# Performance work log

Hardware: AMD Instinct MI355X
Metric: run time of the kernel (lower is better)

The kernel has to match this reference:

```python
import jax, jax.numpy as jnp
import numpy as np
import math

B, L = 32, 1000
N_CHAR, EMB, D_MODEL, N_HEADS, PRED_HS, N_OUT = 256, 512, 512, 8, 512, 8
D_HEAD = D_MODEL // N_HEADS


def _pos_encoding(seq_len, d_model, dtype=jnp.float32):
    pos = jnp.arange(seq_len, dtype=dtype)[:, None]                      # [L,1]
    div = jnp.exp(jnp.arange(0, d_model, 2, dtype=dtype) * (-math.log(10000.0) / d_model))
    pe = jnp.zeros((seq_len, d_model), dtype=dtype)
    pe = pe.at[:, 0::2].set(jnp.sin(pos * div))
    pe = pe.at[:, 1::2].set(jnp.cos(pos * div))
    return pe                                                            # [L,D]


def setup_inputs() -> dict:
    key = jax.random.key(0)
    ks = jax.random.split(key, 12)
    def xavier(k, shape):
        fan_in, fan_out = shape[1], shape[0]
        lim = math.sqrt(6.0 / (fan_in + fan_out))
        return jax.random.uniform(k, shape, jnp.float32, -lim, lim)
    data = jax.random.randint(ks[0], (B, L), 0, N_CHAR, dtype=jnp.int64)
    lengths = jnp.clip(jax.random.randint(ks[1], (B,), 0, L, dtype=jnp.int64), 1, L)
    emb = jax.random.normal(ks[2], (N_CHAR, EMB), jnp.float32) * math.sqrt(2.0 / (N_CHAR + EMB))
    return {
        'data': data,
        'lengths': lengths,
        'emb': emb,
        'Wq': xavier(ks[3], (D_MODEL, EMB)), 'bq': jnp.zeros((D_MODEL,), jnp.float32),
        'Wk': xavier(ks[4], (D_MODEL, EMB)), 'bk': jnp.zeros((D_MODEL,), jnp.float32),
        'Wv': xavier(ks[5], (D_MODEL, EMB)), 'bv': jnp.zeros((D_MODEL,), jnp.float32),
        'W1': xavier(ks[6], (PRED_HS, D_MODEL)), 'b1': jnp.full((PRED_HS,), 0.01, jnp.float32),
        'W2': xavier(ks[7], (N_OUT, PRED_HS)), 'b2': jnp.full((N_OUT,), 0.01, jnp.float32),
    }


def reference(data, lengths, emb, Wq, bq, Wk, bk, Wv, bv, W1, b1, W2, b2):
    bs, seq = data.shape
    x = emb[data]                                              # [B,L,E]
    x = x + _pos_encoding(seq, x.shape[-1], x.dtype)[None]     # positional encoding
    # q/k/v projections -> [B,L,H,dh]
    q = (x @ Wq.T + bq).reshape(bs, seq, N_HEADS, D_HEAD)
    k = (x @ Wk.T + bk).reshape(bs, seq, N_HEADS, D_HEAD)
    v = (x @ Wv.T + bv).reshape(bs, seq, N_HEADS, D_HEAD)
    scale = 1.0 / math.sqrt(D_HEAD)
    score = jnp.einsum('bqhd,bkhd->bhqk', q, k) * scale        # [B,H,L,L]
    causal = jnp.tril(jnp.ones((seq, seq), dtype=bool))        # True = keep
    score = jnp.where(causal[None, None], score, -jnp.inf)
    attn = jax.nn.softmax(score, axis=-1)
    ctx = jnp.einsum('bhqk,bkhd->bqhd', attn, v).reshape(bs, seq, D_MODEL)
    # take hidden state at last valid position per sequence
    ctx_last = jnp.take_along_axis(ctx, (lengths - 1)[:, None, None].astype(jnp.int32), axis=1)[:, 0]  # [B,D]
    h = jax.nn.leaky_relu(ctx_last @ W1.T + b1)                # pred layer 1
    out = jax.nn.relu(h @ W2.T + b2)                           # [B,8]
    out = jnp.mean(out, axis=-1)                               # [B]
    return jax.nn.leaky_relu(out)
```

## Files before the change

### kernel.cpp

```cpp
#include <hip/hip_runtime.h>
#include <math.h>

#define BATCH   32
#define LSEQ    1000
#define LPAD    1024
#define NHEADS  8
#define DHEAD   64

typedef __attribute__((ext_vector_type(8))) short s8v;
typedef __attribute__((ext_vector_type(4))) float f4v;

__device__ __forceinline__ unsigned short f2bf(float f) {
  unsigned u = __builtin_bit_cast(unsigned, f);
  u += 0x7fffu + ((u >> 16) & 1u);
  return (unsigned short)(u >> 16);
}
__device__ __forceinline__ float bf2f(unsigned short h) {
  return __builtin_bit_cast(float, ((unsigned)h) << 16);
}
__device__ __forceinline__ void g2lds16(const void* g, void* l) {
  __builtin_amdgcn_global_load_lds((const __attribute__((address_space(1))) void*)g,
                                   (__attribute__((address_space(3))) void*)l,
                                   16, 0, 0);
}

__global__ __launch_bounds__(256) void prep_kernel(
    const float* __restrict__ Wk, const float* __restrict__ bk,
    const float* __restrict__ Wv, const float* __restrict__ bv,
    unsigned short* __restrict__ Bkv, float* __restrict__ bias_kv) {
  int idx = blockIdx.x * 256 + threadIdx.x;
  int off = idx * 4;
  const float* s = (off < 262144) ? (Wk + off) : (Wv + off - 262144);
  float4 v = *(const float4*)s;
  unsigned r0 = (unsigned)f2bf(v.x) | ((unsigned)f2bf(v.y) << 16);
  unsigned r1 = (unsigned)f2bf(v.z) | ((unsigned)f2bf(v.w) << 16);
  uint2 pk; pk.x = r0; pk.y = r1;
  *(uint2*)(Bkv + off) = pk;
  if (idx < 1024) bias_kv[idx] = (idx < 512) ? bk[idx] : bv[idx - 512];
}

__global__ __launch_bounds__(256) void build_x_kernel(
    const int* __restrict__ data, const int* __restrict__ lengths,
    const float* __restrict__ emb, unsigned short* __restrict__ X) {
  int t    = threadIdx.x;
  int row  = blockIdx.x * 4 + (t >> 6);
  int b    = row / 1000;
  int j    = row - b * 1000;
  int p    = lengths[b] - 1;
  if (j > p) return;
  int lane = t & 63;
  int e0   = lane * 8;
  int tok  = data[row];
  const float* ev = emb + (size_t)tok * 512 + e0;
  float4 a = *(const float4*)(ev);
  float4 c = *(const float4*)(ev + 4);
  float vals[8] = {a.x, a.y, a.z, a.w, c.x, c.y, c.z, c.w};
  #pragma unroll
  for (int i = 0; i < 8; i += 2) {
    int e = e0 + i;
    float dv  = __expf((float)e * (-9.210340371976184f / 512.0f));
    float arg = (float)j * dv;
    vals[i]     += __sinf(arg);
    vals[i + 1] += __cosf(arg);
  }
  unsigned w0 = (unsigned)f2bf(vals[0]) | ((unsigned)f2bf(vals[1]) << 16);
  unsigned w1 = (unsigned)f2bf(vals[2]) | ((unsigned)f2bf(vals[3]) << 16);
  unsigned w2 = (unsigned)f2bf(vals[4]) | ((unsigned)f2bf(vals[5]) << 16);
  unsigned w3 = (unsigned)f2bf(vals[6]) | ((unsigned)f2bf(vals[7]) << 16);
  uint4 pk; pk.x = w0; pk.y = w1; pk.z = w2; pk.w = w3;
  *(uint4*)(X + ((size_t)(b * LPAD + j)) * 512 + e0) = pk;
}

__global__ __launch_bounds__(256) void kv_gemm_kernel(
    const unsigned short* __restrict__ X, const unsigned short* __restrict__ Bkv,
    const float* __restrict__ bias_kv, const int* __restrict__ lengths,
    unsigned short* __restrict__ Ck, unsigned short* __restrict__ Cv) {
  int b    = blockIdx.z;
  int row0 = blockIdx.y * 128;
  int p    = lengths[b] - 1;
  if (row0 > p) return;
  int n0   = blockIdx.x * 128;

  __shared__ unsigned short lA[128 * 64];
  __shared__ unsigned short lB[128 * 64];

  int t = threadIdx.x;
  int w = t >> 6;
  int lane = t & 63;
  int wm = w & 1, wn = w >> 1;

  f4v acc[4][4];
  f4v z = {0.0f, 0.0f, 0.0f, 0.0f};
  #pragma unroll
  for (int i = 0; i < 4; ++i)
    #pragma unroll
    for (int jn = 0; jn < 4; ++jn) acc[i][jn] = z;

  const unsigned short* gA[4];
  const unsigned short* gB[4];
  #pragma unroll
  for (int i = 0; i < 4; ++i) {
    int chunk = (i * 4 + w) * 64 + lane;
    int r  = chunk >> 3;
    int cc = (chunk & 7) ^ (r & 7);
    gA[i] = X   + ((size_t)(b * LPAD + row0 + r)) * 512 + cc * 8;
    gB[i] = Bkv + ((size_t)(n0 + r)) * 512 + cc * 8;
  }

  int q  = lane >> 4;
  int ml = lane & 15;

  for (int kt = 0; kt < 8; ++kt) {
    #pragma unroll
    for (int i = 0; i < 4; ++i) {
      g2lds16(gA[i] + kt * 64, lA + (i * 4 + w) * 512);
      g2lds16(gB[i] + kt * 64, lB + (i * 4 + w) * 512);
    }
    __syncthreads();
    #pragma unroll
    for (int kk = 0; kk < 2; ++kk) {
      s8v af[4], bfr[4];
      #pragma unroll
      for (int mb = 0; mb < 4; ++mb) {
        int m  = wm * 64 + mb * 16 + ml;
        int ch = m * 8 + ((kk * 4 + q) ^ (m & 7));
        af[mb] = *(const s8v*)(&lA[ch * 8]);
      }
      #pragma unroll
      for (int nb = 0; nb < 4; ++nb) {
        int n  = wn * 64 + nb * 16 + ml;
        int ch = n * 8 + ((kk * 4 + q) ^ (n & 7));
        bfr[nb] = *(const s8v*)(&lB[ch * 8]);
      }
      #pragma unroll
      for (int mb = 0; mb < 4; ++mb)
        #pragma unroll
        for (int nb = 0; nb < 4; ++nb)
          acc[mb][nb] = __builtin_amdgcn_mfma_f32_16x16x32_bf16(
              af[mb], bfr[nb], acc[mb][nb], 0, 0, 0);
    }
    __syncthreads();
  }

  bool isK = (n0 < 512);
  unsigned short* Cout = isK ? Ck : Cv;
  int nbase = isK ? n0 : (n0 - 512);
  #pragma unroll
  for (int mb = 0; mb < 4; ++mb) {
    int row = row0 + wm * 64 + mb * 16 + q * 4;
    #pragma unroll
    for (int nb = 0; nb < 4; ++nb) {
      int col = nbase + wn * 64 + nb * 16 + ml;
      int hh = col >> 6, d = col & 63;
      float bias = bias_kv[isK ? col : col + 512];
      size_t baseo = ((size_t)(b * NHEADS + hh) * LPAD + row) * 64 + d;
      #pragma unroll
      for (int r2 = 0; r2 < 4; ++r2)
        Cout[baseo + (size_t)r2 * 64] = f2bf(acc[mb][nb][r2] + bias);
    }
  }
}

__global__ __launch_bounds__(256) void q_proj_kernel(
    const unsigned short* __restrict__ X, const int* __restrict__ lengths,
    const float* __restrict__ Wq, const float* __restrict__ bq,
    float* __restrict__ qout) {
  int chunk = blockIdx.x, b = blockIdx.y;
  int p = lengths[b] - 1;
  int t = threadIdx.x;
  __shared__ float xs[512];
  __shared__ float red[256];
  const unsigned short* xr = X + ((size_t)(b * LPAD + p)) * 512;
  xs[t]       = bf2f(xr[t]);
  xs[t + 256] = bf2f(xr[t + 256]);
  __syncthreads();
  int col = chunk * 64 + (t & 63);
  int kp  = t >> 6;
  const float* wr = Wq + (size_t)col * 512 + kp * 128;
  const float* xp = xs + kp * 128;
  float a = 0.0f;
  for (int e = 0; e < 128; e += 4) {
    float4 wv = *(const float4*)(wr + e);
    a += wv.x * xp[e] + wv.y * xp[e + 1] + wv.z * xp[e + 2] + wv.w * xp[e + 3];
  }
  red[t] = a;
  __syncthreads();
  if (t < 64)
    qout[b * 512 + chunk * 64 + t] =
        red[t] + red[t + 64] + red[t + 128] + red[t + 192] + bq[chunk * 64 + t];
}

__global__ __launch_bounds__(128) void attn_part_kernel(
    const float* __restrict__ qv, const unsigned short* __restrict__ Ck,
    const unsigned short* __restrict__ Cv, const int* __restrict__ lengths,
    float* __restrict__ part) {
  int c = blockIdx.x, h = blockIdx.y, b = blockIdx.z;
  int n_keys = lengths[b];
  int j0 = c * 128;
  if (j0 >= n_keys) return;
  int t = threadIdx.x;
  __shared__ float qs[64];
  __shared__ float redm[2];
  __shared__ float reds[2];
  __shared__ float probs[128];
  __shared__ float ored[128];
  if (t < 64) qs[t] = qv[b * 512 + h * 64 + t] * 0.125f;
  __syncthreads();
  int bh = b * NHEADS + h;
  int j = j0 + t;
  bool valid = j < n_keys;
  const unsigned short* kr = Ck + ((size_t)bh * LPAD + j) * 64;
  float s = 0.0f;
  #pragma unroll
  for (int e = 0; e < 64; e += 8) {
    uint4 u = *(const uint4*)(kr + e);
    unsigned uu[4] = {u.x, u.y, u.z, u.w};
    #pragma unroll
    for (int wi = 0; wi < 4; ++wi) {
      float lo = __builtin_bit_cast(float, uu[wi] << 16);
      float hi = __builtin_bit_cast(float, uu[wi] & 0xffff0000u);
      s += lo * qs[e + wi * 2] + hi * qs[e + wi * 2 + 1];
    }
  }
  float sc = valid ? s : -INFINITY;
  float wm = sc;
  #pragma unroll
  for (int o = 32; o > 0; o >>= 1) wm = fmaxf(wm, __shfl_xor(wm, o, 64));
  if ((t & 63) == 0) redm[t >> 6] = wm;
  __syncthreads();
  float m = fmaxf(redm[0], redm[1]);
  float pp = valid ? __expf(s - m) : 0.0f;
  probs[t] = pp;
  float ws_ = pp;
  #pragma unroll
  for (int o = 32; o > 0; o >>= 1) ws_ += __shfl_xor(ws_, o, 64);
  if ((t & 63) == 0) reds[t >> 6] = ws_;
  __syncthreads();
  int lane = t & 63, w = t >> 6;
  const unsigned short* vr = Cv + ((size_t)bh * LPAD + j0) * 64 + lane;
  float a = 0.0f;
  for (int jl = w; jl < 128; jl += 2)
    a += probs[jl] * bf2f(vr[(size_t)jl * 64]);
  ored[t] = a;
  __syncthreads();
  size_t pi = ((size_t)bh * 8 + c) * 66;
  if (t < 64) part[pi + 2 + t] = ored[t] + ored[t + 64];
  if (t == 0) { part[pi] = m; part[pi + 1] = reds[0] + reds[1]; }
}

__global__ __launch_bounds__(64) void attn_combine_kernel(
    const float* __restrict__ part, const int* __restrict__ lengths,
    float* __restrict__ ctx) {
  int h = blockIdx.x, b = blockIdx.y;
  int t = threadIdx.x;
  int n_keys = lengths[b];
  int nc = (n_keys + 127) >> 7;
  size_t base = ((size_t)(b * NHEADS + h)) * 8 * 66;
  float M = -INFINITY;
  for (int c2 = 0; c2 < nc; ++c2) M = fmaxf(M, part[base + c2 * 66]);
  float S = 0.0f, O = 0.0f;
  for (int c2 = 0; c2 < nc; ++c2) {
    float wv = __expf(part[base + c2 * 66] - M);
    S += wv * part[base + c2 * 66 + 1];
    O += wv * part[base + c2 * 66 + 2 + t];
  }
  ctx[b * 512 + h * 64 + t] = O / S;
}

__global__ __launch_bounds__(256) void mlp1_kernel(
    const float* __restrict__ ctx, const float* __restrict__ W1,
    const float* __restrict__ b1, float* __restrict__ hs) {
  int chunk = blockIdx.x, b = blockIdx.y;
  int t = threadIdx.x;
  __shared__ float xs[512];
  __shared__ float red[256];
  xs[t]       = ctx[b * 512 + t];
  xs[t + 256] = ctx[b * 512 + t + 256];
  __syncthreads();
  int col = chunk * 64 + (t & 63);
  int kp  = t >> 6;
  const float* wr = W1 + (size_t)col * 512 + kp * 128;
  const float* xp = xs + kp * 128;
  float a = 0.0f;
  for (int e = 0; e < 128; e += 4) {
    float4 wv = *(const float4*)(wr + e);
    a += wv.x * xp[e] + wv.y * xp[e + 1] + wv.z * xp[e + 2] + wv.w * xp[e + 3];
  }
  red[t] = a;
  __syncthreads();
  if (t < 64) {
    float v = red[t] + red[t + 64] + red[t + 128] + red[t + 192] + b1[chunk * 64 + t];
    hs[b * 512 + chunk * 64 + t] = (v > 0.0f) ? v : 0.01f * v;
  }
}

__global__ __launch_bounds__(256) void mlp2_kernel(
    const float* __restrict__ hs, const float* __restrict__ W2,
    const float* __restrict__ b2, float* __restrict__ out) {
  int b = blockIdx.x, t = threadIdx.x;
  __shared__ float o8[8];
  int j = t >> 5, sub = t & 31;
  const float* hr  = hs + (size_t)b * 512;
  const float* w2r = W2 + (size_t)j * 512;
  float part = 0.0f;
  for (int e = sub * 16; e < sub * 16 + 16; e += 4) {
    float4 wv = *(const float4*)(w2r + e);
    float4 hv = *(const float4*)(hr + e);
    part += wv.x * hv.x + wv.y * hv.y + wv.z * hv.z + wv.w * hv.w;
  }
  #pragma unroll
  for (int o = 16; o > 0; o >>= 1) part += __shfl_xor(part, o, 64);
  if (sub == 0) o8[j] = fmaxf(part + b2[j], 0.0f);
  __syncthreads();
  if (t == 0) {
    float m = 0.0f;
    #pragma unroll
    for (int i = 0; i < 8; ++i) m += o8[i];
    m *= 0.125f;
    out[b] = (m > 0.0f) ? m : 0.01f * m;
  }
}

extern "C" void kernel_launch(void* const* d_in, const int* in_sizes, int n_in,
                              void* d_out, int out_size, void* d_ws, size_t ws_size,
                              hipStream_t stream) {
  const int*   data    = (const int*)d_in[0];
  const int*   lengths = (const int*)d_in[1];
  const float* emb     = (const float*)d_in[2];
  const float* Wq      = (const float*)d_in[3];
  const float* bq      = (const float*)d_in[4];
  const float* Wk      = (const float*)d_in[5];
  const float* bk      = (const float*)d_in[6];
  const float* Wv      = (const float*)d_in[7];
  const float* bv      = (const float*)d_in[8];
  const float* W1      = (const float*)d_in[9];
  const float* b1      = (const float*)d_in[10];
  const float* W2      = (const float*)d_in[11];
  const float* b2      = (const float*)d_in[12];
  float* out = (float*)d_out;

  char* ws = (char*)d_ws;
  unsigned short* X    = (unsigned short*)(ws);
  unsigned short* Ck   = (unsigned short*)(ws + 33554432);
  unsigned short* Cv   = (unsigned short*)(ws + 67108864);
  unsigned short* Bkv  = (unsigned short*)(ws + 100663296);
  float* bias_kv       = (float*)(ws + 101711872);
  float* qv            = (float*)(ws + 101715968);
  float* ctx           = (float*)(ws + 101781504);
  float* part          = (float*)(ws + 101847040);
  float* hs            = (float*)(ws + 102387712);

  prep_kernel<<<512, 256, 0, stream>>>(Wk, bk, Wv, bv, Bkv, bias_kv);
  build_x_kernel<<<8000, 256, 0, stream>>>(data, lengths, emb, X);
  dim3 g3(8, 8, BATCH);
  kv_gemm_kernel<<<g3, 256, 0, stream>>>(X, Bkv, bias_kv, lengths, Ck, Cv);
  dim3 g4(8, BATCH);
  q_proj_kernel<<<g4, 256, 0, stream>>>(X, lengths, Wq, bq, qv);
  dim3 g5(8, NHEADS, BATCH);
  attn_part_kernel<<<g5, 128, 0, stream>>>(qv, Ck, Cv, lengths, part);
  dim3 g6(NHEADS, BATCH);
  attn_combine_kernel<<<g6, 64, 0, stream>>>(part, lengths, ctx);
  dim3 g7(8, BATCH);
  mlp1_kernel<<<g7, 256, 0, stream>>>(ctx, W1, b1, hs);
  mlp2_kernel<<<BATCH, 256, 0, stream>>>(hs, W2, b2, out);
}
```

Baseline: 173.7 us.

## Fuse q·K scoring into KV GEMM epilogue and merge small kernels

Computes the q projection before the K/V GEMM so that the K-half blocks reduce their accumulator tiles against q directly and write per-key scores instead of storing a bf16 K tensor. Attention then reads one scalar score per key rather than 64 bf16 values. The prep and embedding-build kernels are merged into one launch, and the attention combine step is folded into the first MLP kernel, cutting two launches and the K round-trip through memory. The trade-offs are extra shuffle reductions in the GEMM epilogue and combine work that is repeated across each of the MLP chunk blocks.

```diff
diff --git a/kernel.cpp b/kernel.cpp
--- a/kernel.cpp
+++ b/kernel.cpp
@@ -24,26 +24,26 @@
                                    16, 0, 0);
 }
 
-__global__ __launch_bounds__(256) void prep_kernel(
+__global__ __launch_bounds__(256) void prep_build_kernel(
     const float* __restrict__ Wk, const float* __restrict__ bk,
     const float* __restrict__ Wv, const float* __restrict__ bv,
-    unsigned short* __restrict__ Bkv, float* __restrict__ bias_kv) {
-  int idx = blockIdx.x * 256 + threadIdx.x;
-  int off = idx * 4;
-  const float* s = (off < 262144) ? (Wk + off) : (Wv + off - 262144);
-  float4 v = *(const float4*)s;
-  unsigned r0 = (unsigned)f2bf(v.x) | ((unsigned)f2bf(v.y) << 16);
-  unsigned r1 = (unsigned)f2bf(v.z) | ((unsigned)f2bf(v.w) << 16);
-  uint2 pk; pk.x = r0; pk.y = r1;
-  *(uint2*)(Bkv + off) = pk;
-  if (idx < 1024) bias_kv[idx] = (idx < 512) ? bk[idx] : bv[idx - 512];
-}
-
-__global__ __launch_bounds__(256) void build_x_kernel(
+    unsigned short* __restrict__ Bkv, float* __restrict__ bias_kv,
     const int* __restrict__ data, const int* __restrict__ lengths,
     const float* __restrict__ emb, unsigned short* __restrict__ X) {
-  int t    = threadIdx.x;
-  int row  = blockIdx.x * 4 + (t >> 6);
+  int t = threadIdx.x;
+  if (blockIdx.x < 512) {
+    int idx = blockIdx.x * 256 + t;
+    int off = idx * 4;
+    const float* s = (off < 262144) ? (Wk + off) : (Wv + off - 262144);
+    float4 v = *(const float4*)s;
+    unsigned r0 = (unsigned)f2bf(v.x) | ((unsigned)f2bf(v.y) << 16);
+    unsigned r1 = (unsigned)f2bf(v.z) | ((unsigned)f2bf(v.w) << 16);
+    uint2 pk; pk.x = r0; pk.y = r1;
+    *(uint2*)(Bkv + off) = pk;
+    if (idx < 1024) bias_kv[idx] = (idx < 512) ? bk[idx] : bv[idx - 512];
+    return;
+  }
+  int row  = (blockIdx.x - 512) * 4 + (t >> 6);
   int b    = row / 1000;
   int j    = row - b * 1000;
   int p    = lengths[b] - 1;
@@ -71,101 +71,12 @@
   *(uint4*)(X + ((size_t)(b * LPAD + j)) * 512 + e0) = pk;
 }
 
-__global__ __launch_bounds__(256) void kv_gemm_kernel(
-    const unsigned short* __restrict__ X, const unsigned short* __restrict__ Bkv,
-    const float* __restrict__ bias_kv, const int* __restrict__ lengths,
-    unsigned short* __restrict__ Ck, unsigned short* __restrict__ Cv) {
-  int b    = blockIdx.z;
-  int row0 = blockIdx.y * 128;
-  int p    = lengths[b] - 1;
-  if (row0 > p) return;
-  int n0   = blockIdx.x * 128;
-
-  __shared__ unsigned short lA[128 * 64];
-  __shared__ unsigned short lB[128 * 64];
-
-  int t = threadIdx.x;
-  int w = t >> 6;
-  int lane = t & 63;
-  int wm = w & 1, wn = w >> 1;
-
-  f4v acc[4][4];
-  f4v z = {0.0f, 0.0f, 0.0f, 0.0f};
-  #pragma unroll
-  for (int i = 0; i < 4; ++i)
-    #pragma unroll
-    for (int jn = 0; jn < 4; ++jn) acc[i][jn] = z;
-
-  const unsigned short* gA[4];
-  const unsigned short* gB[4];
-  #pragma unroll
-  for (int i = 0; i < 4; ++i) {
-    int chunk = (i * 4 + w) * 64 + lane;
-    int r  = chunk >> 3;
-    int cc = (chunk & 7) ^ (r & 7);
-    gA[i] = X   + ((size_t)(b * LPAD + row0 + r)) * 512 + cc * 8;
-    gB[i] = Bkv + ((size_t)(n0 + r)) * 512 + cc * 8;
-  }
-
-  int q  = lane >> 4;
-  int ml = lane & 15;
-
-  for (int kt = 0; kt < 8; ++kt) {
-    #pragma unroll
-    for (int i = 0; i < 4; ++i) {
-      g2lds16(gA[i] + kt * 64, lA + (i * 4 + w) * 512);
-      g2lds16(gB[i] + kt * 64, lB + (i * 4 + w) * 512);
-    }
-    __syncthreads();
-    #pragma unroll
-    for (int kk = 0; kk < 2; ++kk) {
-      s8v af[4], bfr[4];
-      #pragma unroll
-      for (int mb = 0; mb < 4; ++mb) {
-        int m  = wm * 64 + mb * 16 + ml;
-        int ch = m * 8 + ((kk * 4 + q) ^ (m & 7));
-        af[mb] = *(const s8v*)(&lA[ch * 8]);
-      }
-      #pragma unroll
-      for (int nb = 0; nb < 4; ++nb) {
-        int n  = wn * 64 + nb * 16 + ml;
-        int ch = n * 8 + ((kk * 4 + q) ^ (n & 7));
-        bfr[nb] = *(const s8v*)(&lB[ch * 8]);
-      }
-      #pragma unroll
-      for (int mb = 0; mb < 4; ++mb)
-        #pragma unroll
-        for (int nb = 0; nb < 4; ++nb)
-          acc[mb][nb] = __builtin_amdgcn_mfma_f32_16x16x32_bf16(
-              af[mb], bfr[nb], acc[mb][nb], 0, 0, 0);
-    }
-    __syncthreads();
-  }
-
-  bool isK = (n0 < 512);
-  unsigned short* Cout = isK ? Ck : Cv;
-  int nbase = isK ? n0 : (n0 - 512);
-  #pragma unroll
-  for (int mb = 0; mb < 4; ++mb) {
-    int row = row0 + wm * 64 + mb * 16 + q * 4;
-    #pragma unroll
-    for (int nb = 0; nb < 4; ++nb) {
-      int col = nbase + wn * 64 + nb * 16 + ml;
-      int hh = col >> 6, d = col & 63;
-      float bias = bias_kv[isK ? col : col + 512];
-      size_t baseo = ((size_t)(b * NHEADS + hh) * LPAD + row) * 64 + d;
-      #pragma unroll
-      for (int r2 = 0; r2 < 4; ++r2)
-        Cout[baseo + (size_t)r2 * 64] = f2bf(acc[mb][nb][r2] + bias);
-    }
-  }
-}
-
 __global__ __launch_bounds__(256) void q_proj_kernel(
     const unsigned short* __restrict__ X, const int* __restrict__ lengths,
     const float* __restrict__ Wq, const float* __restrict__ bq,
-    float* __restrict__ qout) {
-  int chunk = blockIdx.x, b = blockIdx.y;
+    const float* __restrict__ bk,
+    float* __restrict__ qv, float* __restrict__ bias_dot) {
+  int h = blockIdx.x, b = blockIdx.y;
   int p = lengths[b] - 1;
   int t = threadIdx.x;
   __shared__ float xs[512];
@@ -174,7 +85,7 @@
   xs[t]       = bf2f(xr[t]);
   xs[t + 256] = bf2f(xr[t + 256]);
   __syncthreads();
-  int col = chunk * 64 + (t & 63);
+  int col = h * 64 + (t & 63);
   int kp  = t >> 6;
   const float* wr = Wq + (size_t)col * 512 + kp * 128;
   const float* xp = xs + kp * 128;
@@ -185,43 +96,149 @@
   }
   red[t] = a;
   __syncthreads();
-  if (t < 64)
-    qout[b * 512 + chunk * 64 + t] =
-        red[t] + red[t + 64] + red[t + 128] + red[t + 192] + bq[chunk * 64 + t];
+  if (t < 64) {
+    float qval = (red[t] + red[t + 64] + red[t + 128] + red[t + 192]
+                  + bq[h * 64 + t]) * 0.125f;
+    qv[b * 512 + h * 64 + t] = qval;
+    float bd = qval * bk[h * 64 + t];
+    #pragma unroll
+    for (int o = 32; o > 0; o >>= 1) bd += __shfl_xor(bd, o, 64);
+    if (t == 0) bias_dot[b * NHEADS + h] = bd;
+  }
+}
+
+__global__ __launch_bounds__(256) void kv_gemm_kernel(
+    const unsigned short* __restrict__ X, const unsigned short* __restrict__ Bkv,
+    const float* __restrict__ bias_kv, const int* __restrict__ lengths,
+    const float* __restrict__ qv, const float* __restrict__ bias_dot,
+    float* __restrict__ scores, unsigned short* __restrict__ Cv) {
+  int b    = blockIdx.z;
+  int row0 = blockIdx.y * 128;
+  int p    = lengths[b] - 1;
+  if (row0 > p) return;
+  int n0   = blockIdx.x * 128;
+
+  __shared__ unsigned short lA[128 * 64];
+  __shared__ unsigned short lB[128 * 64];
+
+  int t = threadIdx.x;
+  int w = t >> 6;
+  int lane = t & 63;
+  int wm = w & 1, wn = w >> 1;
+
+  f4v acc[4][4];
+  f4v z = {0.0f, 0.0f, 0.0f, 0.0f};
+  #pragma unroll
+  for (int i = 0; i < 4; ++i)
+    #pragma unroll
+    for (int jn = 0; jn < 4; ++jn) acc[i][jn] = z;
+
+  const unsigned short* gA[4];
+  const unsigned short* gB[4];
+  #pragma unroll
+  for (int i = 0; i < 4; ++i) {
+    int chunk = (i * 4 + w) * 64 + lane;
+    int r  = chunk >> 3;
+    int cc = (chunk & 7) ^ (r & 7);
+    gA[i] = X   + ((size_t)(b * LPAD + row0 + r)) * 512 + cc * 8;
+    gB[i] = Bkv + ((size_t)(n0 + r)) * 512 + cc * 8;
+  }
+
+  int q  = lane >> 4;
+  int ml = lane & 15;
+
+  for (int kt = 0; kt < 8; ++kt) {
+    #pragma unroll
+    for (int i = 0; i < 4; ++i) {
+      g2lds16(gA[i] + kt * 64, lA + (i * 4 + w) * 512);
+      g2lds16(gB[i] + kt * 64, lB + (i * 4 + w) * 512);
+    }
+    __syncthreads();
+    #pragma unroll
+    for (int kk = 0; kk < 2; ++kk) {
+      s8v af[4], bfr[4];
+      #pragma unroll
+      for (int mb = 0; mb < 4; ++mb) {
+        int m  = wm * 64 + mb * 16 + ml;
+        int ch = m * 8 + ((kk * 4 + q) ^ (m & 7));
+        af[mb] = *(const s8v*)(&lA[ch * 8]);
+      }
+      #pragma unroll
+      for (int nb = 0; nb < 4; ++nb) {
+        int n  = wn * 64 + nb * 16 + ml;
+        int ch = n * 8 + ((kk * 4 + q) ^ (n & 7));
+        bfr[nb] = *(const s8v*)(&lB[ch * 8]);
+      }
+      #pragma unroll
+      for (int mb = 0; mb < 4; ++mb)
+        #pragma unroll
+        for (int nb = 0; nb < 4; ++nb)
+          acc[mb][nb] = __builtin_amdgcn_mfma_f32_16x16x32_bf16(
+              af[mb], bfr[nb], acc[mb][nb], 0, 0, 0);
+    }
+    __syncthreads();
+  }
+
+  if (blockIdx.x < 4) {
+    int h = blockIdx.x * 2 + wn;
+    float qsv[4];
+    #pragma unroll
+    for (int nb = 0; nb < 4; ++nb)
+      qsv[nb] = qv[b * 512 + h * 64 + nb * 16 + ml];
+    float bd = bias_dot[b * NHEADS + h];
+    size_t sbase = ((size_t)(b * NHEADS + h)) * LPAD + row0 + wm * 64;
+    #pragma unroll
+    for (int mb = 0; mb < 4; ++mb) {
+      float pr[4];
+      #pragma unroll
+      for (int r2 = 0; r2 < 4; ++r2) {
+        float sum = acc[mb][0][r2] * qsv[0] + acc[mb][1][r2] * qsv[1]
+                  + acc[mb][2][r2] * qsv[2] + acc[mb][3][r2] * qsv[3];
+        #pragma unroll
+        for (int o = 1; o < 16; o <<= 1) sum += __shfl_xor(sum, o, 64);
+        pr[r2] = sum;
+      }
+      if (ml == 0) {
+        size_t sb = sbase + mb * 16 + q * 4;
+        #pragma unroll
+        for (int r2 = 0; r2 < 4; ++r2) scores[sb + r2] = pr[r2] + bd;
+      }
+    }
+  } else {
+    int nbase = n0 - 512;
+    #pragma unroll
+    for (int mb = 0; mb < 4; ++mb) {
+      int row = row0 + wm * 64 + mb * 16 + q * 4;
+      #pragma unroll
+      for (int nb = 0; nb < 4; ++nb) {
+        int col = nbase + wn * 64 + nb * 16 + ml;
+        int hh = col >> 6, d = col & 63;
+        float bias = bias_kv[col + 512];
+        size_t baseo = ((size_t)(b * NHEADS + hh) * LPAD + row) * 64 + d;
+        #pragma unroll
+        for (int r2 = 0; r2 < 4; ++r2)
+          Cv[baseo + (size_t)r2 * 64] = f2bf(acc[mb][nb][r2] + bias);
+      }
+    }
+  }
 }
 
 __global__ __launch_bounds__(128) void attn_part_kernel(
-    const float* __restrict__ qv, const unsigned short* __restrict__ Ck,
-    const unsigned short* __restrict__ Cv, const int* __restrict__ lengths,
-    float* __restrict__ part) {
+    const float* __restrict__ scores, const unsigned short* __restrict__ Cv,
+    const int* __restrict__ lengths, float* __restrict__ part) {
   int c = blockIdx.x, h = blockIdx.y, b = blockIdx.z;
   int n_keys = lengths[b];
   int j0 = c * 128;
   if (j0 >= n_keys) return;
   int t = threadIdx.x;
-  __shared__ float qs[64];
   __shared__ float redm[2];
   __shared__ float reds[2];
   __shared__ float probs[128];
   __shared__ float ored[128];
-  if (t < 64) qs[t] = qv[b * 512 + h * 64 + t] * 0.125f;
-  __syncthreads();
   int bh = b * NHEADS + h;
   int j = j0 + t;
   bool valid = j < n_keys;
-  const unsigned short* kr = Ck + ((size_t)bh * LPAD + j) * 64;
-  float s = 0.0f;
-  #pragma unroll
-  for (int e = 0; e < 64; e += 8) {
-    uint4 u = *(const uint4*)(kr + e);
-    unsigned uu[4] = {u.x, u.y, u.z, u.w};
-    #pragma unroll
-    for (int wi = 0; wi < 4; ++wi) {
-      float lo = __builtin_bit_cast(float, uu[wi] << 16);
-      float hi = __builtin_bit_cast(float, uu[wi] & 0xffff0000u);
-      s += lo * qs[e + wi * 2] + hi * qs[e + wi * 2 + 1];
-    }
-  }
+  float s = scores[(size_t)bh * LPAD + j];
   float sc = valid ? s : -INFINITY;
   float wm = sc;
   #pragma unroll
@@ -248,34 +265,31 @@
   if (t == 0) { part[pi] = m; part[pi + 1] = reds[0] + reds[1]; }
 }
 
-__global__ __launch_bounds__(64) void attn_combine_kernel(
+__global__ __launch_bounds__(256) void mlp1_kernel(
     const float* __restrict__ part, const int* __restrict__ lengths,
-    float* __restrict__ ctx) {
-  int h = blockIdx.x, b = blockIdx.y;
-  int t = threadIdx.x;
+    const float* __restrict__ W1, const float* __restrict__ b1,
+    float* __restrict__ hs) {
+  int chunk = blockIdx.x, b = blockIdx.y;
+  int t = threadIdx.x;
+  __shared__ float xs[512];
+  __shared__ float red[256];
   int n_keys = lengths[b];
   int nc = (n_keys + 127) >> 7;
-  size_t base = ((size_t)(b * NHEADS + h)) * 8 * 66;
-  float M = -INFINITY;
-  for (int c2 = 0; c2 < nc; ++c2) M = fmaxf(M, part[base + c2 * 66]);
-  float S = 0.0f, O = 0.0f;
-  for (int c2 = 0; c2 < nc; ++c2) {
-    float wv = __expf(part[base + c2 * 66] - M);
-    S += wv * part[base + c2 * 66 + 1];
-    O += wv * part[base + c2 * 66 + 2 + t];
-  }
-  ctx[b * 512 + h * 64 + t] = O / S;
-}
-
-__global__ __launch_bounds__(256) void mlp1_kernel(
-    const float* __restrict__ ctx, const float* __restrict__ W1,
-    const float* __restrict__ b1, float* __restrict__ hs) {
-  int chunk = blockIdx.x, b = blockIdx.y;
-  int t = threadIdx.x;
-  __shared__ float xs[512];
-  __shared__ float red[256];
-  xs[t]       = ctx[b * 512 + t];
-  xs[t + 256] = ctx[b * 512 + t + 256];
+  #pragma unroll
+  for (int half = 0; half < 2; ++half) {
+    int idx = half * 256 + t;
+    int h = idx >> 6, d = idx & 63;
+    size_t base = ((size_t)(b * NHEADS + h)) * 8 * 66;
+    float M = -INFINITY;
+    for (int c2 = 0; c2 < nc; ++c2) M = fmaxf(M, part[base + c2 * 66]);
+    float S = 0.0f, O = 0.0f;
+    for (int c2 = 0; c2 < nc; ++c2) {
+      float wv = __expf(part[base + c2 * 66] - M);
+      S += wv * part[base + c2 * 66 + 1];
+      O += wv * part[base + c2 * 66 + 2 + d];
+    }
+    xs[idx] = O / S;
+  }
   __syncthreads();
   int col = chunk * 64 + (t & 63);
   int kp  = t >> 6;
@@ -341,26 +355,25 @@
 
   char* ws = (char*)d_ws;
   unsigned short* X    = (unsigned short*)(ws);
-  unsigned short* Ck   = (unsigned short*)(ws + 33554432);
-  unsigned short* Cv   = (unsigned short*)(ws + 67108864);
-  unsigned short* Bkv  = (unsigned short*)(ws + 100663296);
-  float* bias_kv       = (float*)(ws + 101711872);
-  float* qv            = (float*)(ws + 101715968);
-  float* ctx           = (float*)(ws + 101781504);
-  float* part          = (float*)(ws + 101847040);
-  float* hs            = (float*)(ws + 102387712);
-
-  prep_kernel<<<512, 256, 0, stream>>>(Wk, bk, Wv, bv, Bkv, bias_kv);
-  build_x_kernel<<<8000, 256, 0, stream>>>(data, lengths, emb, X);
+  unsigned short* Cv   = (unsigned short*)(ws + 33554432);
+  unsigned short* Bkv  = (unsigned short*)(ws + 67108864);
+  float* bias_kv       = (float*)(ws + 68157440);
+  float* qv            = (float*)(ws + 68161536);
+  float* bias_dot      = (float*)(ws + 68227072);
+  float* scores        = (float*)(ws + 68228096);
+  float* part          = (float*)(ws + 69276672);
+  float* hs            = (float*)(ws + 69817344);
+
+  prep_build_kernel<<<8512, 256, 0, stream>>>(Wk, bk, Wv, bv, Bkv, bias_kv,
+                                              data, lengths, emb, X);
+  dim3 g2(NHEADS, BATCH);
+  q_proj_kernel<<<g2, 256, 0, stream>>>(X, lengths, Wq, bq, bk, qv, bias_dot);
   dim3 g3(8, 8, BATCH);
-  kv_gemm_kernel<<<g3, 256, 0, stream>>>(X, Bkv, bias_kv, lengths, Ck, Cv);
-  dim3 g4(8, BATCH);
-  q_proj_kernel<<<g4, 256, 0, stream>>>(X, lengths, Wq, bq, qv);
-  dim3 g5(8, NHEADS, BATCH);
-  attn_part_kernel<<<g5, 128, 0, stream>>>(qv, Ck, Cv, lengths, part);
-  dim3 g6(NHEADS, BATCH);
-  attn_combine_kernel<<<g6, 64, 0, stream>>>(part, lengths, ctx);
-  dim3 g7(8, BATCH);
-  mlp1_kernel<<<g7, 256, 0, stream>>>(ctx, W1, b1, hs);
+  kv_gemm_kernel<<<g3, 256, 0, stream>>>(X, Bkv, bias_kv, lengths, qv, bias_dot,
+                                         scores, Cv);
+  dim3 g4(8, NHEADS, BATCH);
+  attn_part_kernel<<<g4, 128, 0, stream>>>(scores, Cv, lengths, part);
+  dim3 g5(8, BATCH);
+  mlp1_kernel<<<g5, 256, 0, stream>>>(part, lengths, W1, b1, hs);
   mlp2_kernel<<<BATCH, 256, 0, stream>>>(hs, W2, b2, out);
 }
```

New measurement: 168.2 us. -3.2%, faster.

## Fold Wq/Wk into per-head query vector and apply Wv after attention pooling

Applied to the files above, without the earlier changes.

Drops the full K/V projection GEMM over all tokens. The query is folded through Wk into a per-(batch, head) 512-wide vector, so scores become dot products directly against the embedded inputs X. Softmax-weighted sums of X are then formed per head, and Wv plus its bias is applied once to the pooled vector. This removes the large MFMA GEMM and the K/V writes, at the cost of more small kernels and fp32 CUDA-core dot products that read X for scores and again for pooling.

```diff
diff --git a/kernel.cpp b/kernel.cpp
--- a/kernel.cpp
+++ b/kernel.cpp
@@ -7,9 +7,6 @@
 #define NHEADS  8
 #define DHEAD   64
 
-typedef __attribute__((ext_vector_type(8))) short s8v;
-typedef __attribute__((ext_vector_type(4))) float f4v;
-
 __device__ __forceinline__ unsigned short f2bf(float f) {
   unsigned u = __builtin_bit_cast(unsigned, f);
   u += 0x7fffu + ((u >> 16) & 1u);
@@ -17,26 +14,6 @@
 }
 __device__ __forceinline__ float bf2f(unsigned short h) {
   return __builtin_bit_cast(float, ((unsigned)h) << 16);
-}
-__device__ __forceinline__ void g2lds16(const void* g, void* l) {
-  __builtin_amdgcn_global_load_lds((const __attribute__((address_space(1))) void*)g,
-                                   (__attribute__((address_space(3))) void*)l,
-                                   16, 0, 0);
-}
-
-__global__ __launch_bounds__(256) void prep_kernel(
-    const float* __restrict__ Wk, const float* __restrict__ bk,
-    const float* __restrict__ Wv, const float* __restrict__ bv,
-    unsigned short* __restrict__ Bkv, float* __restrict__ bias_kv) {
-  int idx = blockIdx.x * 256 + threadIdx.x;
-  int off = idx * 4;
-  const float* s = (off < 262144) ? (Wk + off) : (Wv + off - 262144);
-  float4 v = *(const float4*)s;
-  unsigned r0 = (unsigned)f2bf(v.x) | ((unsigned)f2bf(v.y) << 16);
-  unsigned r1 = (unsigned)f2bf(v.z) | ((unsigned)f2bf(v.w) << 16);
-  uint2 pk; pk.x = r0; pk.y = r1;
-  *(uint2*)(Bkv + off) = pk;
-  if (idx < 1024) bias_kv[idx] = (idx < 512) ? bk[idx] : bv[idx - 512];
 }
 
 __global__ __launch_bounds__(256) void build_x_kernel(
@@ -71,113 +48,203 @@
   *(uint4*)(X + ((size_t)(b * LPAD + j)) * 512 + e0) = pk;
 }
 
-__global__ __launch_bounds__(256) void kv_gemm_kernel(
-    const unsigned short* __restrict__ X, const unsigned short* __restrict__ Bkv,
-    const float* __restrict__ bias_kv, const int* __restrict__ lengths,
-    unsigned short* __restrict__ Ck, unsigned short* __restrict__ Cv) {
-  int b    = blockIdx.z;
-  int row0 = blockIdx.y * 128;
-  int p    = lengths[b] - 1;
-  if (row0 > p) return;
-  int n0   = blockIdx.x * 128;
-
-  __shared__ unsigned short lA[128 * 64];
-  __shared__ unsigned short lB[128 * 64];
-
-  int t = threadIdx.x;
-  int w = t >> 6;
-  int lane = t & 63;
-  int wm = w & 1, wn = w >> 1;
-
-  f4v acc[4][4];
-  f4v z = {0.0f, 0.0f, 0.0f, 0.0f};
-  #pragma unroll
-  for (int i = 0; i < 4; ++i)
-    #pragma unroll
-    for (int jn = 0; jn < 4; ++jn) acc[i][jn] = z;
-
-  const unsigned short* gA[4];
-  const unsigned short* gB[4];
-  #pragma unroll
-  for (int i = 0; i < 4; ++i) {
-    int chunk = (i * 4 + w) * 64 + lane;
-    int r  = chunk >> 3;
-    int cc = (chunk & 7) ^ (r & 7);
-    gA[i] = X   + ((size_t)(b * LPAD + row0 + r)) * 512 + cc * 8;
-    gB[i] = Bkv + ((size_t)(n0 + r)) * 512 + cc * 8;
-  }
-
-  int q  = lane >> 4;
-  int ml = lane & 15;
-
-  for (int kt = 0; kt < 8; ++kt) {
-    #pragma unroll
-    for (int i = 0; i < 4; ++i) {
-      g2lds16(gA[i] + kt * 64, lA + (i * 4 + w) * 512);
-      g2lds16(gB[i] + kt * 64, lB + (i * 4 + w) * 512);
-    }
-    __syncthreads();
-    #pragma unroll
-    for (int kk = 0; kk < 2; ++kk) {
-      s8v af[4], bfr[4];
-      #pragma unroll
-      for (int mb = 0; mb < 4; ++mb) {
-        int m  = wm * 64 + mb * 16 + ml;
-        int ch = m * 8 + ((kk * 4 + q) ^ (m & 7));
-        af[mb] = *(const s8v*)(&lA[ch * 8]);
-      }
-      #pragma unroll
-      for (int nb = 0; nb < 4; ++nb) {
-        int n  = wn * 64 + nb * 16 + ml;
-        int ch = n * 8 + ((kk * 4 + q) ^ (n & 7));
-        bfr[nb] = *(const s8v*)(&lB[ch * 8]);
-      }
-      #pragma unroll
-      for (int mb = 0; mb < 4; ++mb)
-        #pragma unroll
-        for (int nb = 0; nb < 4; ++nb)
-          acc[mb][nb] = __builtin_amdgcn_mfma_f32_16x16x32_bf16(
-              af[mb], bfr[nb], acc[mb][nb], 0, 0, 0);
-    }
-    __syncthreads();
-  }
-
-  bool isK = (n0 < 512);
-  unsigned short* Cout = isK ? Ck : Cv;
-  int nbase = isK ? n0 : (n0 - 512);
-  #pragma unroll
-  for (int mb = 0; mb < 4; ++mb) {
-    int row = row0 + wm * 64 + mb * 16 + q * 4;
-    #pragma unroll
-    for (int nb = 0; nb < 4; ++nb) {
-      int col = nbase + wn * 64 + nb * 16 + ml;
-      int hh = col >> 6, d = col & 63;
-      float bias = bias_kv[isK ? col : col + 512];
-      size_t baseo = ((size_t)(b * NHEADS + hh) * LPAD + row) * 64 + d;
-      #pragma unroll
-      for (int r2 = 0; r2 < 4; ++r2)
-        Cout[baseo + (size_t)r2 * 64] = f2bf(acc[mb][nb][r2] + bias);
-    }
-  }
-}
-
-__global__ __launch_bounds__(256) void q_proj_kernel(
+__global__ __launch_bounds__(256) void qfold_kernel(
     const unsigned short* __restrict__ X, const int* __restrict__ lengths,
     const float* __restrict__ Wq, const float* __restrict__ bq,
-    float* __restrict__ qout) {
-  int chunk = blockIdx.x, b = blockIdx.y;
+    const float* __restrict__ Wk, const float* __restrict__ bk,
+    float* __restrict__ wfold, float* __restrict__ bias_dot) {
+  int h = blockIdx.x, b = blockIdx.y;
   int p = lengths[b] - 1;
   int t = threadIdx.x;
   __shared__ float xs[512];
   __shared__ float red[256];
+  __shared__ float qs[64];
   const unsigned short* xr = X + ((size_t)(b * LPAD + p)) * 512;
   xs[t]       = bf2f(xr[t]);
   xs[t + 256] = bf2f(xr[t + 256]);
   __syncthreads();
-  int col = chunk * 64 + (t & 63);
+  int col = h * 64 + (t & 63);
   int kp  = t >> 6;
-  const float* wr = Wq + (size_t)col * 512 + kp * 128;
-  const float* xp = xs + kp * 128;
+  {
+    const float* wr = Wq + (size_t)col * 512 + kp * 128;
+    const float* xp = xs + kp * 128;
+    float a = 0.0f;
+    for (int e = 0; e < 128; e += 4) {
+      float4 wv = *(const float4*)(wr + e);
+      a += wv.x * xp[e] + wv.y * xp[e + 1] + wv.z * xp[e + 2] + wv.w * xp[e + 3];
+    }
+    red[t] = a;
+  }
+  __syncthreads();
+  if (t < 64) {
+    float qval = (red[t] + red[t + 64] + red[t + 128] + red[t + 192]
+                  + bq[h * 64 + t]) * 0.125f;
+    qs[t] = qval;
+    float bd = qval * bk[h * 64 + t];
+    #pragma unroll
+    for (int o = 32; o > 0; o >>= 1) bd += __shfl_xor(bd, o, 64);
+    if (t == 0) bias_dot[b * NHEADS + h] = bd;
+  }
+  __syncthreads();
+  float a0 = 0.0f, a1 = 0.0f;
+  const float* wkb = Wk + (size_t)(h * 64) * 512;
+  for (int d = 0; d < 64; ++d) {
+    float qd = qs[d];
+    a0 += qd * wkb[d * 512 + t];
+    a1 += qd * wkb[d * 512 + t + 256];
+  }
+  size_t wb = ((size_t)(b * NHEADS + h)) * 512;
+  wfold[wb + t]       = a0;
+  wfold[wb + t + 256] = a1;
+}
+
+__global__ __launch_bounds__(256) void score_kernel(
+    const unsigned short* __restrict__ X, const float* __restrict__ wfold,
+    const float* __restrict__ bias_dot, const int* __restrict__ lengths,
+    float* __restrict__ scores) {
+  int b = blockIdx.y;
+  int n_keys = lengths[b];
+  int row0 = blockIdx.x * 16;
+  if (row0 >= n_keys) return;
+  int t = threadIdx.x;
+  int w = t >> 6, lane = t & 63;
+  float wf[8][8];
+  float bd[8];
+  size_t wbase = ((size_t)b * NHEADS) * 512 + lane * 8;
+  #pragma unroll
+  for (int h = 0; h < 8; ++h) {
+    float4 u0 = *(const float4*)(wfold + wbase + h * 512);
+    float4 u1 = *(const float4*)(wfold + wbase + h * 512 + 4);
+    wf[h][0] = u0.x; wf[h][1] = u0.y; wf[h][2] = u0.z; wf[h][3] = u0.w;
+    wf[h][4] = u1.x; wf[h][5] = u1.y; wf[h][6] = u1.z; wf[h][7] = u1.w;
+    bd[h] = bias_dot[b * NHEADS + h];
+  }
+  #pragma unroll
+  for (int r = 0; r < 4; ++r) {
+    int j = row0 + r * 4 + w;
+    if (j >= n_keys) continue;
+    const unsigned short* xr = X + ((size_t)(b * LPAD + j)) * 512 + lane * 8;
+    uint4 u = *(const uint4*)xr;
+    unsigned uu[4] = {u.x, u.y, u.z, u.w};
+    float xf[8];
+    #pragma unroll
+    for (int wi = 0; wi < 4; ++wi) {
+      xf[wi * 2]     = __builtin_bit_cast(float, uu[wi] << 16);
+      xf[wi * 2 + 1] = __builtin_bit_cast(float, uu[wi] & 0xffff0000u);
+    }
+    #pragma unroll
+    for (int h = 0; h < 8; ++h) {
+      float s = xf[0] * wf[h][0] + xf[1] * wf[h][1] + xf[2] * wf[h][2]
+              + xf[3] * wf[h][3] + xf[4] * wf[h][4] + xf[5] * wf[h][5]
+              + xf[6] * wf[h][6] + xf[7] * wf[h][7];
+      #pragma unroll
+      for (int o = 1; o < 64; o <<= 1) s += __shfl_xor(s, o, 64);
+      if (lane == 0)
+        scores[((size_t)(b * NHEADS + h)) * LPAD + j] = s + bd[h];
+    }
+  }
+}
+
+__global__ __launch_bounds__(256) void softmax_kernel(
+    const float* __restrict__ scores, const int* __restrict__ lengths,
+    float* __restrict__ probs, float* __restrict__ sums) {
+  int h = blockIdx.x, b = blockIdx.y;
+  int n = lengths[b];
+  int t = threadIdx.x;
+  __shared__ float red[4];
+  size_t base = ((size_t)(b * NHEADS + h)) * LPAD;
+  float lm = -INFINITY;
+  for (int j = t; j < n; j += 256) lm = fmaxf(lm, scores[base + j]);
+  #pragma unroll
+  for (int o = 32; o > 0; o >>= 1) lm = fmaxf(lm, __shfl_xor(lm, o, 64));
+  if ((t & 63) == 0) red[t >> 6] = lm;
+  __syncthreads();
+  float gmax = fmaxf(fmaxf(red[0], red[1]), fmaxf(red[2], red[3]));
+  __syncthreads();
+  float ls = 0.0f;
+  for (int j = t; j < n; j += 256) {
+    float e = __expf(scores[base + j] - gmax);
+    probs[base + j] = e;
+    ls += e;
+  }
+  #pragma unroll
+  for (int o = 32; o > 0; o >>= 1) ls += __shfl_xor(ls, o, 64);
+  if ((t & 63) == 0) red[t >> 6] = ls;
+  __syncthreads();
+  if (t == 0) sums[b * NHEADS + h] = red[0] + red[1] + red[2] + red[3];
+}
+
+__global__ __launch_bounds__(256) void ypass_kernel(
+    const unsigned short* __restrict__ X, const float* __restrict__ probs,
+    const int* __restrict__ lengths, float* __restrict__ y_part) {
+  int jc = blockIdx.x, b = blockIdx.y;
+  int n_keys = lengths[b];
+  int j0 = jc * 256;
+  if (j0 >= n_keys) return;
+  int cnt = min(256, n_keys - j0);
+  int t = threadIdx.x;
+  __shared__ float pl[8][256];
+  #pragma unroll
+  for (int h = 0; h < 8; ++h)
+    pl[h][t] = (t < cnt) ? probs[((size_t)(b * NHEADS + h)) * LPAD + j0 + t] : 0.0f;
+  __syncthreads();
+  int w = t >> 6, lane = t & 63;
+  float acc[8][8];
+  #pragma unroll
+  for (int h = 0; h < 8; ++h)
+    #pragma unroll
+    for (int i = 0; i < 8; ++i) acc[h][i] = 0.0f;
+  for (int jj = w; jj < cnt; jj += 4) {
+    const unsigned short* xr = X + ((size_t)(b * LPAD + j0 + jj)) * 512 + lane * 8;
+    uint4 u = *(const uint4*)xr;
+    unsigned uu[4] = {u.x, u.y, u.z, u.w};
+    float xf[8];
+    #pragma unroll
+    for (int wi = 0; wi < 4; ++wi) {
+      xf[wi * 2]     = __builtin_bit_cast(float, uu[wi] << 16);
+      xf[wi * 2 + 1] = __builtin_bit_cast(float, uu[wi] & 0xffff0000u);
+    }
+    #pragma unroll
+    for (int h = 0; h < 8; ++h) {
+      float pj = pl[h][jj];
+      #pragma unroll
+      for (int i = 0; i < 8; ++i) acc[h][i] += pj * xf[i];
+    }
+  }
+  size_t sb = (((size_t)(b * 4 + jc)) * 4 + w) * (8 * 512) + lane * 8;
+  #pragma unroll
+  for (int h = 0; h < 8; ++h)
+    #pragma unroll
+    for (int i = 0; i < 8; ++i) y_part[sb + h * 512 + i] = acc[h][i];
+}
+
+__global__ __launch_bounds__(256) void ctx_kernel(
+    const float* __restrict__ y_part, const float* __restrict__ sums,
+    const int* __restrict__ lengths, const float* __restrict__ Wv,
+    const float* __restrict__ bv, float* __restrict__ ctx) {
+  int h = blockIdx.x, b = blockIdx.y;
+  int t = threadIdx.x;
+  __shared__ float ys[512];
+  __shared__ float red[256];
+  int n_keys = lengths[b];
+  int nc = (n_keys + 255) >> 8;
+  float inv = 1.0f / sums[b * NHEADS + h];
+  float s0 = 0.0f, s1 = 0.0f;
+  for (int jc = 0; jc < nc; ++jc) {
+    #pragma unroll
+    for (int w = 0; w < 4; ++w) {
+      size_t sb = (((size_t)(b * 4 + jc)) * 4 + w) * (8 * 512) + h * 512;
+      s0 += y_part[sb + t];
+      s1 += y_part[sb + t + 256];
+    }
+  }
+  ys[t]       = s0 * inv;
+  ys[t + 256] = s1 * inv;
+  __syncthreads();
+  int col = h * 64 + (t & 63);
+  int kp  = t >> 6;
+  const float* wr = Wv + (size_t)col * 512 + kp * 128;
+  const float* xp = ys + kp * 128;
   float a = 0.0f;
   for (int e = 0; e < 128; e += 4) {
     float4 wv = *(const float4*)(wr + e);
@@ -186,85 +253,8 @@
   red[t] = a;
   __syncthreads();
   if (t < 64)
-    qout[b * 512 + chunk * 64 + t] =
-        red[t] + red[t + 64] + red[t + 128] + red[t + 192] + bq[chunk * 64 + t];
-}
-
-__global__ __launch_bounds__(128) void attn_part_kernel(
-    const float* __restrict__ qv, const unsigned short* __restrict__ Ck,
-    const unsigned short* __restrict__ Cv, const int* __restrict__ lengths,
-    float* __restrict__ part) {
-  int c = blockIdx.x, h = blockIdx.y, b = blockIdx.z;
-  int n_keys = lengths[b];
-  int j0 = c * 128;
-  if (j0 >= n_keys) return;
-  int t = threadIdx.x;
-  __shared__ float qs[64];
-  __shared__ float redm[2];
-  __shared__ float reds[2];
-  __shared__ float probs[128];
-  __shared__ float ored[128];
-  if (t < 64) qs[t] = qv[b * 512 + h * 64 + t] * 0.125f;
-  __syncthreads();
-  int bh = b * NHEADS + h;
-  int j = j0 + t;
-  bool valid = j < n_keys;
-  const unsigned short* kr = Ck + ((size_t)bh * LPAD + j) * 64;
-  float s = 0.0f;
-  #pragma unroll
-  for (int e = 0; e < 64; e += 8) {
-    uint4 u = *(const uint4*)(kr + e);
-    unsigned uu[4] = {u.x, u.y, u.z, u.w};
-    #pragma unroll
-    for (int wi = 0; wi < 4; ++wi) {
-      float lo = __builtin_bit_cast(float, uu[wi] << 16);
-      float hi = __builtin_bit_cast(float, uu[wi] & 0xffff0000u);
-      s += lo * qs[e + wi * 2] + hi * qs[e + wi * 2 + 1];
-    }
-  }
-  float sc = valid ? s : -INFINITY;
-  float wm = sc;
-  #pragma unroll
-  for (int o = 32; o > 0; o >>= 1) wm = fmaxf(wm, __shfl_xor(wm, o, 64));
-  if ((t & 63) == 0) redm[t >> 6] = wm;
-  __syncthreads();
-  float m = fmaxf(redm[0], redm[1]);
-  float pp = valid ? __expf(s - m) : 0.0f;
-  probs[t] = pp;
-  float ws_ = pp;
-  #pragma unroll
-  for (int o = 32; o > 0; o >>= 1) ws_ += __shfl_xor(ws_, o, 64);
-  if ((t & 63) == 0) reds[t >> 6] = ws_;
-  __syncthreads();
-  int lane = t & 63, w = t >> 6;
-  const unsigned short* vr = Cv + ((size_t)bh * LPAD + j0) * 64 + lane;
-  float a = 0.0f;
-  for (int jl = w; jl < 128; jl += 2)
-    a += probs[jl] * bf2f(vr[(size_t)jl * 64]);
-  ored[t] = a;
-  __syncthreads();
-  size_t pi = ((size_t)bh * 8 + c) * 66;
-  if (t < 64) part[pi + 2 + t] = ored[t] + ored[t + 64];
-  if (t == 0) { part[pi] = m; part[pi + 1] = reds[0] + reds[1]; }
-}
-
-__global__ __launch_bounds__(64) void attn_combine_kernel(
-    const float* __restrict__ part, const int* __restrict__ lengths,
-    float* __restrict__ ctx) {
-  int h = blockIdx.x, b = blockIdx.y;
-  int t = threadIdx.x;
-  int n_keys = lengths[b];
-  int nc = (n_keys + 127) >> 7;
-  size_t base = ((size_t)(b * NHEADS + h)) * 8 * 66;
-  float M = -INFINITY;
-  for (int c2 = 0; c2 < nc; ++c2) M = fmaxf(M, part[base + c2 * 66]);
-  float S = 0.0f, O = 0.0f;
-  for (int c2 = 0; c2 < nc; ++c2) {
-    float wv = __expf(part[base + c2 * 66] - M);
-    S += wv * part[base + c2 * 66 + 1];
-    O += wv * part[base + c2 * 66 + 2 + t];
-  }
-  ctx[b * 512 + h * 64 + t] = O / S;
+    ctx[b * 512 + h * 64 + t] =
+        red[t] + red[t + 64] + red[t + 128] + red[t + 192] + bv[h * 64 + t];
 }
 
 __global__ __launch_bounds__(256) void mlp1_kernel(
@@ -340,26 +330,27 @@
   float* out = (float*)d_out;
 
   char* ws = (char*)d_ws;
-  unsigned short* X    = (unsigned short*)(ws);
-  unsigned short* Ck   = (unsigned short*)(ws + 33554432);
-  unsigned short* Cv   = (unsigned short*)(ws + 67108864);
-  unsigned short* Bkv  = (unsigned short*)(ws + 100663296);
-  float* bias_kv       = (float*)(ws + 101711872);
-  float* qv            = (float*)(ws + 101715968);
-  float* ctx           = (float*)(ws + 101781504);
-  float* part          = (float*)(ws + 101847040);
-  float* hs            = (float*)(ws + 102387712);
-
-  prep_kernel<<<512, 256, 0, stream>>>(Wk, bk, Wv, bv, Bkv, bias_kv);
+  unsigned short* X = (unsigned short*)(ws);
+  float* wfold      = (float*)(ws + 33554432);
+  float* bias_dot   = (float*)(ws + 34078720);
+  float* scores     = (float*)(ws + 34079744);
+  float* probs      = (float*)(ws + 35128320);
+  float* sums       = (float*)(ws + 36176896);
+  float* y_part     = (float*)(ws + 36177920);
+  float* ctx        = (float*)(ws + 44566528);
+  float* hs         = (float*)(ws + 44632064);
+
   build_x_kernel<<<8000, 256, 0, stream>>>(data, lengths, emb, X);
-  dim3 g3(8, 8, BATCH);
-  kv_gemm_kernel<<<g3, 256, 0, stream>>>(X, Bkv, bias_kv, lengths, Ck, Cv);
-  dim3 g4(8, BATCH);
-  q_proj_kernel<<<g4, 256, 0, stream>>>(X, lengths, Wq, bq, qv);
-  dim3 g5(8, NHEADS, BATCH);
-  attn_part_kernel<<<g5, 128, 0, stream>>>(qv, Ck, Cv, lengths, part);
+  dim3 g2(NHEADS, BATCH);
+  qfold_kernel<<<g2, 256, 0, stream>>>(X, lengths, Wq, bq, Wk, bk, wfold, bias_dot);
+  dim3 g3(63, BATCH);
+  score_kernel<<<g3, 256, 0, stream>>>(X, wfold, bias_dot, lengths, scores);
+  dim3 g4(NHEADS, BATCH);
+  softmax_kernel<<<g4, 256, 0, stream>>>(scores, lengths, probs, sums);
+  dim3 g5(4, BATCH);
+  ypass_kernel<<<g5, 256, 0, stream>>>(X, probs, lengths, y_part);
   dim3 g6(NHEADS, BATCH);
-  attn_combine_kernel<<<g6, 64, 0, stream>>>(part, lengths, ctx);
+  ctx_kernel<<<g6, 256, 0, stream>>>(y_part, sums, lengths, Wv, bv, ctx);
   dim3 g7(8, BATCH);
   mlp1_kernel<<<g7, 256, 0, stream>>>(ctx, W1, b1, hs);
   mlp2_kernel<<<BATCH, 256, 0, stream>>>(hs, W2, b2, out);
```

Result: faster. 155.8 us (-10.3%).
